# Performance work log

Measured on AMD Instinct MI355X. Metric: run time of the kernel, lower is better.

The kernel has to match this reference:

```python
import jax, jax.numpy as jnp
import numpy as np

B, L, KNN = 8, 512, 16
D, H, NL, DLAT = 1024, 16, 2, 64
DH = D // H
DFF = 4 * D
HENC = D // 2          # SwiGLUFFNEncoder hidden = d_model // 2
POS_CLIP = 32
NPOS = 2 * POS_CLIP + 1


def _layernorm(x, g, b, eps=1e-5):
    m = x.mean(-1, keepdims=True)
    v = ((x - m) ** 2).mean(-1, keepdims=True)
    return (x - m) / jnp.sqrt(v + eps) * g + b


def setup_inputs() -> dict:
    key = jax.random.key(0)
    ks = jax.random.split(key, 16)

    def g(i, shape, scale=0.02):
        return jax.random.normal(ks[i], shape, dtype=jnp.float32) * scale

    return {
        "coords": jax.random.normal(ks[0], (B, L, 3, 3), dtype=jnp.float32) * 3.0,
        "eps": jax.random.normal(ks[1], (B, L, DLAT), dtype=jnp.float32),
        "emb": g(2, (NPOS, D)),
        "ln1_g": jnp.ones((NL, D)), "ln1_b": jnp.zeros((NL, D)),
        "Wqkv": g(3, (NL, D, 3 * D)), "bqkv": jnp.zeros((NL, 3 * D)),
        "dist_scale": g(4, (NL, H), 1.0),
        "Wo": g(5, (NL, D, D)), "bo": jnp.zeros((NL, D)),
        "ln2_g": jnp.ones((NL, D)), "ln2_b": jnp.zeros((NL, D)),
        "Wf1": g(6, (NL, D, 2 * DFF)), "bf1": jnp.zeros((NL, 2 * DFF)),
        "Wf2": g(7, (NL, DFF, D)), "bf2": jnp.zeros((NL, D)),
        "lnf_g": jnp.ones((D,)), "lnf_b": jnp.zeros((D,)),
        "We1": g(8, (D, 2 * HENC)), "be1": jnp.zeros((2 * HENC,)),
        "We2": g(9, (HENC, 2 * DLAT)), "be2": jnp.zeros((2 * DLAT,)),
        "attention_mask": jnp.ones((B, L), dtype=bool),
        "sequence_id": jnp.zeros((B, L), dtype=jnp.int32),
    }


def reference(coords, eps, emb, ln1_g, ln1_b, Wqkv, bqkv, dist_scale, Wo, bo,
              ln2_g, ln2_b, Wf1, bf1, Wf2, bf2, lnf_g, lnf_b, We1, be1, We2, be2,
              attention_mask, sequence_id):
    # --- frames: only CA translations feed the geometric attention bias ---
    t = coords[..., 1, :]                       # CA atoms, [B,L,3]

    # --- KNN graph build (no_grad in torch -> stop_gradient) ---
    ca = jax.lax.stop_gradient(t)
    d2 = ((ca[:, :, None, :] - ca[:, None, :, :]) ** 2).sum(-1)   # [B,L,L]
    same_seq = sequence_id[:, :, None] == sequence_id[:, None, :]
    valid = attention_mask[:, None, :] & same_seq
    d2 = jnp.where(valid, d2, jnp.inf)
    _, edges = jax.lax.top_k(-d2, KNN)          # [B,L,KNN]; self is index 0

    def gather(x):  # node_gather: x [B,L,...] -> [B,L,KNN,...]
        return jax.vmap(lambda xb, ib: xb[ib])(x, edges)

    tg = gather(t).reshape(B * L, KNN, 3)                 # neighbor translations
    maskg = gather(attention_mask).reshape(B * L, KNN)

    # --- relative positional embedding (residue_index=None -> knn edges) ---
    res_idxs = edges.reshape(B * L, KNN)
    diff = res_idxs - res_idxs[:, :1]
    z = emb[jnp.clip(diff, -POS_CLIP, POS_CLIP) + POS_CLIP]   # [N,E,D]

    # --- local geometric transformer over the 16-neighbor window ---
    dist = jnp.sqrt(((tg[:, :, None, :] - tg[:, None, :, :]) ** 2).sum(-1) + 1e-8)  # [N,E,E]
    for l in range(NL):
        h = _layernorm(z, ln1_g[l], ln1_b[l])
        qkv = h @ Wqkv[l] + bqkv[l]
        q, k, v = [a.reshape(B * L, KNN, H, DH) for a in jnp.split(qkv, 3, axis=-1)]
        scores = jnp.einsum('nehd,nfhd->nhef', q, k) / np.sqrt(DH).astype(np.float32)
        scores = scores - jax.nn.softplus(dist_scale[l])[None, :, None, None] * dist[:, None]
        scores = jnp.where(maskg[:, None, None, :], scores, -1e9)
        a = jax.nn.softmax(scores, axis=-1)
        o = jnp.einsum('nhef,nfhd->nehd', a, v).reshape(B * L, KNN, D)
        z = z + o @ Wo[l] + bo[l]
        h2 = _layernorm(z, ln2_g[l], ln2_b[l])
        a1, b1 = jnp.split(h2 @ Wf1[l] + bf1[l], 2, axis=-1)
        z = z + (jax.nn.silu(a1) * b1) @ Wf2[l] + bf2[l]

    # --- extract central node, norm, SwiGLU encoder head, reparameterize ---
    zc = z.reshape(B, L, KNN, D)[:, :, 0, :]
    zc = _layernorm(zc, lnf_g, lnf_b)
    zc = jnp.where(attention_mask[..., None], zc, 0.0)
    u1, v1 = jnp.split(zc @ We1 + be1, 2, axis=-1)
    hh = jax.nn.silu(u1) * v1
    mu, logvar = jnp.split(hh @ We2 + be2, 2, axis=-1)
    logvar = jnp.minimum(logvar, 5.0)
    zs = mu + eps * jnp.exp(0.5 * logvar)
    return zs, mu, logvar
```

## Files before the change

kernel.cpp:

```cpp
#include <hip/hip_runtime.h>
#include <hip/hip_bf16.h>
#include <math.h>

#define LLEN 512
#define KNNK 16
#define DIM 1024
#define NHEAD 16
#define NLAYER 2
#define DFFN 4096
#define POSCLIP 32
#define NQ 4096
#define NTOK 65536
#define HSPLIT 4

typedef __attribute__((ext_vector_type(8))) short short8v;
typedef __attribute__((ext_vector_type(4))) float f32x4;
typedef unsigned short ushort_t;

__device__ __forceinline__ float b2f(ushort_t u) {
  union { unsigned u; float f; } x; x.u = ((unsigned)u) << 16; return x.f;
}

__device__ __forceinline__ void xcd_map(int bid, int Mtiles, int Ntiles, int XN,
                                        int& mt, int& nt) {
  int nt_per = Ntiles / XN;
  int mt_per = (Mtiles * XN) >> 3;
  int xcd = bid & 7, i = bid >> 3;
  int xn = xcd % XN, xm = xcd / XN;
  int ntl = i % nt_per, mtl = i / nt_per;
  mt = xm * mt_per + mtl;
  nt = xn * nt_per + ntl;
}

#define GLD16(gp, lp)                                                          \
  __builtin_amdgcn_global_load_lds(                                            \
      (const __attribute__((address_space(1))) void*)(gp),                     \
      (__attribute__((address_space(3))) void*)(lp), 16, 0, 0)

__global__ __launch_bounds__(64) void knn_kernel(const float* __restrict__ coords,
                                                 int* __restrict__ edges) {
  int n = blockIdx.x;
  int b = n / LLEN, i = n % LLEN;
  int lane = threadIdx.x;
  const float* cb = coords + (size_t)b * LLEN * 9;
  float xi = cb[i * 9 + 3], yi = cb[i * 9 + 4], zi = cb[i * 9 + 5];
  float d[8];
#pragma unroll
  for (int r = 0; r < 8; ++r) {
    int j = r * 64 + lane;
    float dx = xi - cb[j * 9 + 3];
    float dy = yi - cb[j * 9 + 4];
    float dz = zi - cb[j * 9 + 5];
    d[r] = dx * dx + dy * dy + dz * dz;
  }
  for (int s = 0; s < KNNK; ++s) {
    float bv = INFINITY; int bi = 1 << 30;
#pragma unroll
    for (int r = 0; r < 8; ++r) {
      int j = r * 64 + lane;
      if (d[r] < bv || (d[r] == bv && j < bi)) { bv = d[r]; bi = j; }
    }
#pragma unroll
    for (int off = 32; off > 0; off >>= 1) {
      float ov = __shfl_xor(bv, off);
      int   oi = __shfl_xor(bi, off);
      if (ov < bv || (ov == bv && oi < bi)) { bv = ov; bi = oi; }
    }
    if (lane == 0) edges[n * KNNK + s] = bi;
    if ((bi & 63) == lane) d[bi >> 6] = INFINITY;
  }
}

__global__ __launch_bounds__(256) void dist_kernel(const float* __restrict__ coords,
                                                   const int* __restrict__ edges,
                                                   float* __restrict__ dist) {
  int n = blockIdx.x; int b = n / LLEN;
  __shared__ float tx[16], ty[16], tz[16];
  int t = threadIdx.x;
  const float* cb = coords + (size_t)b * LLEN * 9;
  if (t < 16) {
    int j = edges[n * KNNK + t];
    tx[t] = cb[j * 9 + 3]; ty[t] = cb[j * 9 + 4]; tz[t] = cb[j * 9 + 5];
  }
  __syncthreads();
  int e = t >> 4, f = t & 15;
  float dx = tx[e] - tx[f], dy = ty[e] - ty[f], dz = tz[e] - tz[f];
  dist[(size_t)n * 256 + t] = sqrtf(dx * dx + dy * dy + dz * dz + 1e-8f);
}

__global__ __launch_bounds__(256) void zinit_kernel(const int* __restrict__ edges,
                                                    const float* __restrict__ emb,
                                                    float* __restrict__ zbuf, int tok0) {
  int tl = blockIdx.x;
  int tok = tok0 + tl;
  int n = tok >> 4;
  int diff = edges[tok] - edges[n << 4];
  int idx = min(max(diff, -POSCLIP), POSCLIP) + POSCLIP;
  ((float4*)(zbuf + (size_t)tl * DIM))[threadIdx.x] =
      ((const float4*)(emb + (size_t)idx * DIM))[threadIdx.x];
}

__global__ __launch_bounds__(256) void ln_kernel(const float* __restrict__ X, int stride,
                                                 const float* __restrict__ g,
                                                 const float* __restrict__ bta,
                                                 __hip_bfloat16* __restrict__ Y) {
  int row = blockIdx.x; int t = threadIdx.x;
  const float4* xr = (const float4*)(X + (size_t)row * stride);
  float4 v = xr[t];
  float s = v.x + v.y + v.z + v.w;
  __shared__ float red[8];
  for (int off = 32; off; off >>= 1) s += __shfl_down(s, off);
  int wid = t >> 6;
  if ((t & 63) == 0) red[wid] = s;
  __syncthreads();
  if (t == 0) red[4] = (red[0] + red[1] + red[2] + red[3]) * (1.0f / DIM);
  __syncthreads();
  float mean = red[4];
  float d0 = v.x - mean, d1 = v.y - mean, d2 = v.z - mean, d3 = v.w - mean;
  float s2 = d0 * d0 + d1 * d1 + d2 * d2 + d3 * d3;
  for (int off = 32; off; off >>= 1) s2 += __shfl_down(s2, off);
  if ((t & 63) == 0) red[wid] = s2;
  __syncthreads();
  if (t == 0) red[5] = rsqrtf((red[0] + red[1] + red[2] + red[3]) * (1.0f / DIM) + 1e-5f);
  __syncthreads();
  float rstd = red[5];
  float4 gv = ((const float4*)g)[t], bv = ((const float4*)bta)[t];
  size_t o = (size_t)row * DIM + t * 4;
  Y[o + 0] = __float2bfloat16(d0 * rstd * gv.x + bv.x);
  Y[o + 1] = __float2bfloat16(d1 * rstd * gv.y + bv.y);
  Y[o + 2] = __float2bfloat16(d2 * rstd * gv.z + bv.z);
  Y[o + 3] = __float2bfloat16(d3 * rstd * gv.w + bv.w);
}

__global__ __launch_bounds__(256) void wconv_kernel(const float* __restrict__ W,
                                                    __hip_bfloat16* __restrict__ Wt,
                                                    int K, int N) {
  __shared__ float tile[32][33];
  int n0 = blockIdx.x * 32, k0 = blockIdx.y * 32;
  int c = threadIdx.x & 31, r = threadIdx.x >> 5;
#pragma unroll
  for (int i = 0; i < 4; ++i)
    tile[r + i * 8][c] = W[(size_t)(k0 + r + i * 8) * N + n0 + c];
  __syncthreads();
#pragma unroll
  for (int i = 0; i < 4; ++i)
    Wt[(size_t)(n0 + r + i * 8) * K + k0 + c] = __float2bfloat16(tile[c][r + i * 8]);
}


template <int MODE>
__global__ __launch_bounds__(256, 3) void gemmT128_kernel(
    const ushort_t* __restrict__ A,
    const ushort_t* __restrict__ Wt,
    const float* __restrict__ bias,
    void* __restrict__ Cout,
    int K, int Mtiles, int Cstride, int Ntiles, int XN) {
  __shared__ ushort_t Alds[3][4096];
  __shared__ ushort_t Blds[3][4096];
  int t = threadIdx.x;
  int w = t >> 6, lane = t & 63;
  int wr = w >> 1, wc = w & 1;
  int fr = lane & 15, kg = lane >> 4;

  int mt, nt;
  xcd_map(blockIdx.x, Mtiles, Ntiles, XN, mt, nt);
  size_t m0 = (size_t)mt * 128, n0 = (size_t)nt * 128;

  int stg_r = w * 16 + (lane >> 2);
  int stg_c = (((lane & 3) ^ ((lane >> 3) & 3)) << 3);
  const ushort_t* gAl = A + (m0 + stg_r) * (size_t)K + stg_c;
  const ushort_t* gBl = Wt + (n0 + stg_r) * (size_t)K + stg_c;
  int lds_w = w * 512;

#define SAt(slot, kcol, j) GLD16(gAl + (size_t)(j) * 64 * K + (kcol), Alds[slot] + (j) * 2048 + lds_w)
#define SBt(slot, kcol, j) GLD16(gBl + (size_t)(j) * 64 * K + (kcol), Blds[slot] + (j) * 2048 + lds_w)

  f32x4 acc[4][4];
#pragma unroll
  for (int i = 0; i < 4; ++i)
#pragma unroll
    for (int j = 0; j < 4; ++j) acc[i][j] = (f32x4){0.f, 0.f, 0.f, 0.f};

  int usw = ((kg ^ ((fr >> 1) & 3)) << 3);

  SAt(0, 0, 0); SAt(0, 0, 1); SBt(0, 0, 0); SBt(0, 0, 1);
  SAt(1, 32, 0); SAt(1, 32, 1); SBt(1, 32, 0); SBt(1, 32, 1);
  asm volatile("s_waitcnt vmcnt(4)" ::: "memory");
  __builtin_amdgcn_s_barrier();

  short8v af[4], bf[4];
  int NT = K >> 5;
  int sl = 0, st = 2;
  for (int ti = 0; ti < NT; ++ti) {
    int kS = (ti + 2) << 5;
    int stg = (ti + 2) < NT;
    const ushort_t* sA = Alds[sl];
    const ushort_t* sB = Blds[sl];
#pragma unroll
    for (int mi = 0; mi < 4; ++mi)
      af[mi] = *(const short8v*)(sA + (wr * 64 + mi * 16 + fr) * 32 + usw);
#pragma unroll
    for (int ni = 0; ni < 4; ++ni)
      bf[ni] = *(const short8v*)(sB + (wc * 64 + ni * 16 + fr) * 32 + usw);
    if (stg) { SAt(st, kS, 0); SAt(st, kS, 1); SBt(st, kS, 0); SBt(st, kS, 1); }
    asm volatile("s_waitcnt lgkmcnt(0)" ::: "memory");
    __builtin_amdgcn_sched_barrier(0);
    __builtin_amdgcn_s_setprio(1);
#pragma unroll
    for (int mi = 0; mi < 4; ++mi)
#pragma unroll
      for (int ni = 0; ni < 4; ++ni)
        acc[mi][ni] = __builtin_amdgcn_mfma_f32_16x16x32_bf16(af[mi], bf[ni], acc[mi][ni], 0, 0, 0);
    __builtin_amdgcn_s_setprio(0);
    if (stg) { asm volatile("s_waitcnt vmcnt(4)" ::: "memory"); }
    else if (ti + 1 < NT) { asm volatile("s_waitcnt vmcnt(0)" ::: "memory"); }
    __builtin_amdgcn_s_barrier();
    sl = (sl == 2) ? 0 : sl + 1;
    st = (st == 2) ? 0 : st + 1;
  }
#undef SAt
#undef SBt

  int er = wr * 64 + (lane >> 4) * 4;
  int ec = wc * 64 + fr;
#pragma unroll
  for (int mi = 0; mi < 4; ++mi) {
#pragma unroll
    for (int ni = 0; ni < 4; ++ni) {
      int col = (int)n0 + ec + ni * 16;
      float bs = bias[col];
#pragma unroll
      for (int j = 0; j < 4; ++j) {
        size_t row = m0 + er + mi * 16 + j;
        size_t cidx = row * (size_t)Cstride + col;
        float x = acc[mi][ni][j] + bs;
        if constexpr (MODE == 0) {
          ((__hip_bfloat16*)Cout)[cidx] = __float2bfloat16(x);
        } else {
          ((float*)Cout)[cidx] += x;
        }
      }
    }
  }
}

__global__ __launch_bounds__(256, 2) void gemmGW_kernel(
    const ushort_t* __restrict__ A,
    const ushort_t* __restrict__ Wt,
    const float* __restrict__ bias,
    __hip_bfloat16* __restrict__ Cout,
    int K, int Mtiles, int Cstride, int NhRows, int Ntiles, int XN) {
  __shared__ ushort_t Alds[3][4096];
  __shared__ ushort_t B1lds[3][4096];
  __shared__ ushort_t B2lds[3][4096];
  int t = threadIdx.x;
  int w = t >> 6, lane = t & 63;
  int wr = w >> 1, wc = w & 1;
  int fr = lane & 15, kg = lane >> 4;

  int mt, nt;
  xcd_map(blockIdx.x, Mtiles, Ntiles, XN, mt, nt);
  size_t m0 = (size_t)mt * 128, n0 = (size_t)nt * 128;

  int stg_r = w * 16 + (lane >> 2);
  int stg_c = (((lane & 3) ^ ((lane >> 3) & 3)) << 3);
  const ushort_t* gAl = A + (m0 + stg_r) * (size_t)K + stg_c;
  const ushort_t* gB1 = Wt + (n0 + stg_r) * (size_t)K + stg_c;
  const ushort_t* gB2 = Wt + ((size_t)NhRows + n0 + stg_r) * (size_t)K + stg_c;
  int lds_w = w * 512;

#define SAg(slot, kcol, j) GLD16(gAl + (size_t)(j) * 64 * K + (kcol), Alds[slot] + (j) * 2048 + lds_w)
#define SB1g(slot, kcol, j) GLD16(gB1 + (size_t)(j) * 64 * K + (kcol), B1lds[slot] + (j) * 2048 + lds_w)
#define SB2g(slot, kcol, j) GLD16(gB2 + (size_t)(j) * 64 * K + (kcol), B2lds[slot] + (j) * 2048 + lds_w)

  f32x4 acc1[4][4], acc2[4][4];
#pragma unroll
  for (int i = 0; i < 4; ++i)
#pragma unroll
    for (int j = 0; j < 4; ++j) {
      acc1[i][j] = (f32x4){0.f, 0.f, 0.f, 0.f};
      acc2[i][j] = (f32x4){0.f, 0.f, 0.f, 0.f};
    }

  int usw = ((kg ^ ((fr >> 1) & 3)) << 3);

  SAg(0, 0, 0); SAg(0, 0, 1); SB1g(0, 0, 0); SB1g(0, 0, 1); SB2g(0, 0, 0); SB2g(0, 0, 1);
  SAg(1, 32, 0); SAg(1, 32, 1); SB1g(1, 32, 0); SB1g(1, 32, 1); SB2g(1, 32, 0); SB2g(1, 32, 1);
  asm volatile("s_waitcnt vmcnt(6)" ::: "memory");
  __builtin_amdgcn_s_barrier();

  short8v af[4], bf1[4], bf2[4];
  int NT = K >> 5;
  int sl = 0, st = 2;
  for (int ti = 0; ti < NT; ++ti) {
    int kS = (ti + 2) << 5;
    int stg = (ti + 2) < NT;
    const ushort_t* sA = Alds[sl];
    const ushort_t* sB1 = B1lds[sl];
    const ushort_t* sB2 = B2lds[sl];
#pragma unroll
    for (int mi = 0; mi < 4; ++mi)
      af[mi] = *(const short8v*)(sA + (wr * 64 + mi * 16 + fr) * 32 + usw);
#pragma unroll
    for (int ni = 0; ni < 4; ++ni) {
      bf1[ni] = *(const short8v*)(sB1 + (wc * 64 + ni * 16 + fr) * 32 + usw);
      bf2[ni] = *(const short8v*)(sB2 + (wc * 64 + ni * 16 + fr) * 32 + usw);
    }
    if (stg) {
      SAg(st, kS, 0); SAg(st, kS, 1);
      SB1g(st, kS, 0); SB1g(st, kS, 1);
      SB2g(st, kS, 0); SB2g(st, kS, 1);
    }
    asm volatile("s_waitcnt lgkmcnt(0)" ::: "memory");
    __builtin_amdgcn_sched_barrier(0);
    __builtin_amdgcn_s_setprio(1);
#pragma unroll
    for (int mi = 0; mi < 4; ++mi)
#pragma unroll
      for (int ni = 0; ni < 4; ++ni) {
        acc1[mi][ni] = __builtin_amdgcn_mfma_f32_16x16x32_bf16(af[mi], bf1[ni], acc1[mi][ni], 0, 0, 0);
        acc2[mi][ni] = __builtin_amdgcn_mfma_f32_16x16x32_bf16(af[mi], bf2[ni], acc2[mi][ni], 0, 0, 0);
      }
    __builtin_amdgcn_s_setprio(0);
    if (stg) { asm volatile("s_waitcnt vmcnt(6)" ::: "memory"); }
    else if (ti + 1 < NT) { asm volatile("s_waitcnt vmcnt(0)" ::: "memory"); }
    __builtin_amdgcn_s_barrier();
    sl = (sl == 2) ? 0 : sl + 1;
    st = (st == 2) ? 0 : st + 1;
  }
#undef SAg
#undef SB1g
#undef SB2g

  int er = wr * 64 + (lane >> 4) * 4;
  int ec = wc * 64 + fr;
#pragma unroll
  for (int mi = 0; mi < 4; ++mi) {
#pragma unroll
    for (int ni = 0; ni < 4; ++ni) {
      int col = (int)n0 + ec + ni * 16;
      float b1v = bias[col];
      float b2v = bias[NhRows + col];
#pragma unroll
      for (int j = 0; j < 4; ++j) {
        size_t row = m0 + er + mi * 16 + j;
        float x1 = acc1[mi][ni][j] + b1v;
        float x2 = acc2[mi][ni][j] + b2v;
        float sg = x1 / (1.f + expf(-x1));
        Cout[row * (size_t)Cstride + col] = __float2bfloat16(sg * x2);
      }
    }
  }
}

template <int MODE>
__global__ __launch_bounds__(256) void mgemm_kernel(
    const __hip_bfloat16* __restrict__ A,
    const __hip_bfloat16* __restrict__ Wt,
    const float* __restrict__ bias,
    void* __restrict__ Cout,
    int K, int Nh, int Cstride) {
  __shared__ ushort_t As[4 * 128 * 8];
  __shared__ ushort_t Bs[4 * 128 * 8];
  __shared__ ushort_t Bs2[(MODE == 2) ? 4 * 128 * 8 : 8];
  int t = threadIdx.x;
  int w = t >> 6, lane = t & 63;
  int wr = w >> 1, wc = w & 1;
  size_t m0 = (size_t)blockIdx.y * 128;
  size_t n0 = (size_t)blockIdx.x * 128;
  int cell0 = w * 64 + lane;
  int cell1 = 256 + w * 64 + lane;
  int kg0 = cell0 >> 7, rw0 = cell0 & 127;
  int kg1 = cell1 >> 7, rw1 = cell1 & 127;
  const ushort_t* gA = (const ushort_t*)A;
  const ushort_t* gB = (const ushort_t*)Wt;
  const ushort_t* gB2 = (const ushort_t*)(Wt + (size_t)Nh * K);
  size_t a0 = (m0 + rw0) * (size_t)K + kg0 * 8;
  size_t a1 = (m0 + rw1) * (size_t)K + kg1 * 8;
  size_t b0 = (n0 + rw0) * (size_t)K + kg0 * 8;
  size_t b1 = (n0 + rw1) * (size_t)K + kg1 * 8;
  int ldso0 = w * 1024;
  int ldso1 = 4096 + w * 1024;
  f32x4 acc[4][4];
  f32x4 acc2[4][4];
#pragma unroll
  for (int i = 0; i < 4; ++i)
#pragma unroll
    for (int j = 0; j < 4; ++j) {
      acc[i][j] = (f32x4){0.f, 0.f, 0.f, 0.f};
      acc2[i][j] = (f32x4){0.f, 0.f, 0.f, 0.f};
    }
  int fr = lane & 15, kg = lane >> 4;
  int abase = (kg * 128 + wr * 64 + fr) * 16;
  int bbase = (kg * 128 + wc * 64 + fr) * 16;
  for (int k0 = 0; k0 < K; k0 += 32) {
    __syncthreads();
    GLD16(gA + a0 + k0, (char*)As + ldso0);
    GLD16(gA + a1 + k0, (char*)As + ldso1);
    GLD16(gB + b0 + k0, (char*)Bs + ldso0);
    GLD16(gB + b1 + k0, (char*)Bs + ldso1);
    if constexpr (MODE == 2) {
      GLD16(gB2 + b0 + k0, (char*)Bs2 + ldso0);
      GLD16(gB2 + b1 + k0, (char*)Bs2 + ldso1);
    }
    __syncthreads();
    short8v a[4], b[4];
#pragma unroll
    for (int mi = 0; mi < 4; ++mi)
      a[mi] = *(const short8v*)((const char*)As + abase + mi * 256);
#pragma unroll
    for (int ni = 0; ni < 4; ++ni)
      b[ni] = *(const short8v*)((const char*)Bs + bbase + ni * 256);
#pragma unroll
    for (int mi = 0; mi < 4; ++mi)
#pragma unroll
      for (int ni = 0; ni < 4; ++ni)
        acc[mi][ni] = __builtin_amdgcn_mfma_f32_16x16x32_bf16(a[mi], b[ni], acc[mi][ni], 0, 0, 0);
    if constexpr (MODE == 2) {
#pragma unroll
      for (int ni = 0; ni < 4; ++ni)
        b[ni] = *(const short8v*)((const char*)Bs2 + bbase + ni * 256);
#pragma unroll
      for (int mi = 0; mi < 4; ++mi)
#pragma unroll
        for (int ni = 0; ni < 4; ++ni)
          acc2[mi][ni] = __builtin_amdgcn_mfma_f32_16x16x32_bf16(a[mi], b[ni], acc2[mi][ni], 0, 0, 0);
    }
  }
  int er = wr * 64 + (lane >> 4) * 4;
  int ec = wc * 64 + fr;
#pragma unroll
  for (int mi = 0; mi < 4; ++mi) {
#pragma unroll
    for (int ni = 0; ni < 4; ++ni) {
      int col = (int)n0 + ec + ni * 16;
      float bs1 = bias[col];
#pragma unroll
      for (int j = 0; j < 4; ++j) {
        size_t row = m0 + er + mi * 16 + j;
        size_t cidx = row * (size_t)Cstride + col;
        float x = acc[mi][ni][j] + bs1;
        if constexpr (MODE == 3) {
          ((float*)Cout)[cidx] = x;
        } else {
          float x2 = acc2[mi][ni][j] + bias[Nh + col];
          float sig = 1.f / (1.f + expf(-x));
          ((__hip_bfloat16*)Cout)[cidx] = __float2bfloat16(x * sig * x2);
        }
      }
    }
  }
}

__global__ __launch_bounds__(256) void attn_g_kernel(const __hip_bfloat16* __restrict__ qkv65,
                                                     const int* __restrict__ edges,
                                                     const float* __restrict__ dist,
                                                     const float* __restrict__ ds_l,
                                                     __hip_bfloat16* __restrict__ o) {
  int nq = blockIdx.x >> 2;
  int h0 = (blockIdx.x & 3) * (NHEAD / HSPLIT);
  int t = threadIdx.x;
  __shared__ float qs[16][65], ks[16][65], vs[16][65];
  __shared__ float sc[16][17], dl[16][17];
  __shared__ float sps_s[NHEAD];
  __shared__ int map_s[16];
  dl[t >> 4][t & 15] = dist[(size_t)nq * 256 + t];
  if (t < NHEAD) sps_s[t] = log1pf(expf(ds_l[t]));
  if (t < 16) {
    int diff = edges[nq * 16 + t] - edges[nq * 16];
    map_s[t] = min(max(diff, -POSCLIP), POSCLIP) + POSCLIP;
  }
  __syncthreads();
  int e = t >> 4, c4 = (t & 15) * 4;
  const ushort_t* qp = (const ushort_t*)qkv65;
  size_t ebase = (size_t)map_s[e] * 3072;
  for (int h = h0; h < h0 + NHEAD / HSPLIT; ++h) {
    const ushort_t* p = qp + ebase + h * 64 + c4;
    ushort4 qv = *(const ushort4*)p;
    ushort4 kv = *(const ushort4*)(p + 1024);
    ushort4 vv = *(const ushort4*)(p + 2048);
    qs[e][c4] = b2f(qv.x); qs[e][c4 + 1] = b2f(qv.y); qs[e][c4 + 2] = b2f(qv.z); qs[e][c4 + 3] = b2f(qv.w);
    ks[e][c4] = b2f(kv.x); ks[e][c4 + 1] = b2f(kv.y); ks[e][c4 + 2] = b2f(kv.z); ks[e][c4 + 3] = b2f(kv.w);
    vs[e][c4] = b2f(vv.x); vs[e][c4 + 1] = b2f(vv.y); vs[e][c4 + 2] = b2f(vv.z); vs[e][c4 + 3] = b2f(vv.w);
    __syncthreads();
    int ee = t >> 4, ff = t & 15;
    float s = 0.f;
#pragma unroll
    for (int d = 0; d < 64; ++d) s = fmaf(qs[ee][d], ks[ff][d], s);
    sc[ee][ff] = s * 0.125f - sps_s[h] * dl[ee][ff];
    __syncthreads();
    if (t < 16) {
      float m = -1e30f;
      for (int f = 0; f < 16; ++f) m = fmaxf(m, sc[t][f]);
      float sum = 0.f;
      for (int f = 0; f < 16; ++f) { float pe = expf(sc[t][f] - m); sc[t][f] = pe; sum += pe; }
      float inv = 1.f / sum;
      for (int f = 0; f < 16; ++f) sc[t][f] *= inv;
    }
    __syncthreads();
#pragma unroll
    for (int r = 0; r < 4; ++r) {
      int idx = t + 256 * r;
      int oe = idx >> 6, od = idx & 63;
      float acc = 0.f;
#pragma unroll
      for (int f = 0; f < 16; ++f) acc = fmaf(sc[oe][f], vs[f][od], acc);
      o[(size_t)(nq * 16 + oe) * 1024 + h * 64 + od] = __float2bfloat16(acc);
    }
    __syncthreads();
  }
}

__global__ __launch_bounds__(256) void attn2_kernel(const __hip_bfloat16* __restrict__ qkv,
                                                    const float* __restrict__ dist,
                                                    const float* __restrict__ ds_l,
                                                    __hip_bfloat16* __restrict__ o) {
  int nq = blockIdx.x;
  int t = threadIdx.x;
  __shared__ ushort_t ks[16 * 1032];
  __shared__ ushort_t vs[16 * 1032];
  __shared__ float qsf[1024];
  __shared__ float sc[16][17];
  __shared__ float pm[16], pi[16], sps_s[16], dl[16];
  const ushort_t* qp = (const ushort_t*)qkv;
  size_t base = (size_t)nq * 16 * 3072;
#pragma unroll
  for (int i = 0; i < 8; ++i) {
    int flat8 = (i * 256 + t) * 8;
    int e = flat8 >> 10, cc = flat8 & 1023;
    *(short8v*)(ks + e * 1032 + cc) = *(const short8v*)(qp + base + (size_t)e * 3072 + 1024 + cc);
    *(short8v*)(vs + e * 1032 + cc) = *(const short8v*)(qp + base + (size_t)e * 3072 + 2048 + cc);
  }
  {
    ushort4 qv = *(const ushort4*)(qp + base + t * 4);
    qsf[t * 4 + 0] = b2f(qv.x); qsf[t * 4 + 1] = b2f(qv.y);
    qsf[t * 4 + 2] = b2f(qv.z); qsf[t * 4 + 3] = b2f(qv.w);
  }
  if (t < 16) {
    sps_s[t] = log1pf(expf(ds_l[t]));
    dl[t] = dist[(size_t)nq * 256 + t];
  }
  __syncthreads();
  int h = t >> 4, f = t & 15;
  float s = 0.f;
#pragma unroll
  for (int dc = 0; dc < 8; ++dc) {
    short8v k8 = *(const short8v*)(ks + f * 1032 + h * 64 + dc * 8);
#pragma unroll
    for (int j = 0; j < 8; ++j)
      s = fmaf(qsf[h * 64 + dc * 8 + j], b2f((ushort_t)k8[j]), s);
  }
  sc[h][f] = s * 0.125f - sps_s[h] * dl[f];
  __syncthreads();
  if (t < 16) {
    float m = -1e30f;
    for (int ff = 0; ff < 16; ++ff) m = fmaxf(m, sc[t][ff]);
    float sum = 0.f;
    for (int ff = 0; ff < 16; ++ff) sum += expf(sc[t][ff] - m);
    pm[t] = m; pi[t] = 1.f / sum;
  }
  __syncthreads();
  float p = expf(sc[h][f] - pm[h]) * pi[h];
  __syncthreads();
  sc[h][f] = p;
  __syncthreads();
#pragma unroll
  for (int r = 0; r < 4; ++r) {
    int idx = t + 256 * r;
    int oh = idx >> 6, od = idx & 63;
    float acc = 0.f;
#pragma unroll
    for (int f2 = 0; f2 < 16; ++f2)
      acc = fmaf(sc[oh][f2], b2f(vs[f2 * 1032 + oh * 64 + od]), acc);
    o[(size_t)nq * 1024 + idx] = __float2bfloat16(acc);
  }
}

__global__ __launch_bounds__(256) void z0copy_kernel(const float* __restrict__ z,
                                                     float* __restrict__ z0) {
  ((float4*)(z0 + (size_t)blockIdx.x * 1024))[threadIdx.x] =
      ((const float4*)(z + (size_t)blockIdx.x * 16384))[threadIdx.x];
}

__global__ __launch_bounds__(64) void final_kernel(const float* __restrict__ tmp,
                                                   const float* __restrict__ eps,
                                                   float* __restrict__ out) {
  int r = blockIdx.x; int j = threadIdx.x;
  float mu = tmp[r * 128 + j];
  float lv = fminf(tmp[r * 128 + 64 + j], 5.0f);
  float zs = mu + eps[r * 64 + j] * expf(0.5f * lv);
  out[r * 64 + j] = zs;
  out[262144 + r * 64 + j] = mu;
  out[524288 + r * 64 + j] = lv;
}

extern "C" void kernel_launch(void* const* d_in, const int* in_sizes, int n_in,
                              void* d_out, int out_size, void* d_ws, size_t ws_size,
                              hipStream_t stream) {
  (void)in_sizes; (void)n_in; (void)out_size;
  const float* coords = (const float*)d_in[0];
  const float* eps    = (const float*)d_in[1];
  const float* emb    = (const float*)d_in[2];
  const float* ln1_g  = (const float*)d_in[3];
  const float* ln1_b  = (const float*)d_in[4];
  const float* Wqkv   = (const float*)d_in[5];
  const float* bqkv   = (const float*)d_in[6];
  const float* dist_scale = (const float*)d_in[7];
  const float* Wo     = (const float*)d_in[8];
  const float* bo     = (const float*)d_in[9];
  const float* ln2_g  = (const float*)d_in[10];
  const float* ln2_b  = (const float*)d_in[11];
  const float* Wf1    = (const float*)d_in[12];
  const float* bf1    = (const float*)d_in[13];
  const float* Wf2    = (const float*)d_in[14];
  const float* bf2    = (const float*)d_in[15];
  const float* lnf_g  = (const float*)d_in[16];
  const float* lnf_b  = (const float*)d_in[17];
  const float* We1    = (const float*)d_in[18];
  const float* be1    = (const float*)d_in[19];
  const float* We2    = (const float*)d_in[20];
  const float* be2    = (const float*)d_in[21];

  char* ws = (char*)d_ws;
  int*   edges = (int*)ws;
  float* dist  = (float*)(ws + (4ull << 20));
  __hip_bfloat16* hfinal = (__hip_bfloat16*)(ws + (8ull << 20));
  __hip_bfloat16* gated  = (__hip_bfloat16*)(ws + (16ull << 20));
  float* tmp   = (float*)(ws + (20ull << 20));
  __hip_bfloat16* o_all  = (__hip_bfloat16*)(ws + (22ull << 20));
  float* z0_all = (float*)(ws + (30ull << 20));
  __hip_bfloat16* wbase = (__hip_bfloat16*)(ws + (46ull << 20));
  size_t woff = 0;
  __hip_bfloat16* wqkvT = wbase + woff; woff += 2ull * 3072 * 1024;
  __hip_bfloat16* woT   = wbase + woff; woff += 2ull * 1024 * 1024;
  __hip_bfloat16* wf1T  = wbase + woff; woff += 2ull * 8192 * 1024;
  __hip_bfloat16* wf2T  = wbase + woff; woff += 2ull * 1024 * 4096;
  __hip_bfloat16* we1T  = wbase + woff; woff += 1024ull * 1024;
  __hip_bfloat16* we2T  = wbase + woff; woff += 128ull * 512;
  __hip_bfloat16* h65   = wbase + woff; woff += 128ull * 1024;
  __hip_bfloat16* qkv65 = wbase + woff; woff += 128ull * 3072;

  const size_t FIXED = 116ull << 20;
  int CQ = 4096;
  while (CQ > 256 && FIXED + (size_t)CQ * 16 * 14336ull > ws_size) CQ >>= 1;
  if (FIXED + (size_t)CQ * 16 * 14336ull > ws_size) return;
  size_t CT = (size_t)CQ * KNNK;
  char* creg = ws + FIXED;
  float* zbuf = (float*)creg;
  __hip_bfloat16* hbuf = (__hip_bfloat16*)(creg + CT * 4096);
  __hip_bfloat16* sh8  = (__hip_bfloat16*)(creg + CT * 6144);
  __hip_bfloat16* h2        = hbuf;
  __hip_bfloat16* gated_all = sh8;

  knn_kernel<<<NQ, 64, 0, stream>>>(coords, edges);
  dist_kernel<<<NQ, 256, 0, stream>>>(coords, edges, dist);
  for (int l = 0; l < NLAYER; ++l) {
    wconv_kernel<<<dim3(96, 32), 256, 0, stream>>>(Wqkv + (size_t)l * 1024 * 3072,
                                                   wqkvT + (size_t)l * 3072 * 1024, 1024, 3072);
    wconv_kernel<<<dim3(32, 32), 256, 0, stream>>>(Wo + (size_t)l * 1024 * 1024,
                                                   woT + (size_t)l * 1024 * 1024, 1024, 1024);
    wconv_kernel<<<dim3(256, 32), 256, 0, stream>>>(Wf1 + (size_t)l * 1024 * 8192,
                                                    wf1T + (size_t)l * 8192 * 1024, 1024, 8192);
    wconv_kernel<<<dim3(32, 128), 256, 0, stream>>>(Wf2 + (size_t)l * 4096 * 1024,
                                                    wf2T + (size_t)l * 1024 * 4096, 4096, 1024);
  }
  wconv_kernel<<<dim3(32, 32), 256, 0, stream>>>(We1, we1T, 1024, 1024);
  wconv_kernel<<<dim3(4, 16), 256, 0, stream>>>(We2, we2T, 512, 128);

  ln_kernel<<<65, 256, 0, stream>>>(emb, DIM, ln1_g, ln1_b, h65);
  gemmT128_kernel<0><<<24, 256, 0, stream>>>(
      (const ushort_t*)h65, (const ushort_t*)wqkvT, bqkv, qkv65, 1024, 1, 3072, 24, 8);

  int NCH = NQ / CQ;
  int MT128 = (int)(CT / 128);
  for (int c = 0; c < NCH; ++c) {
    zinit_kernel<<<(int)CT, 256, 0, stream>>>(edges, emb, zbuf, (int)(c * CT));
    attn_g_kernel<<<CQ * HSPLIT, 256, 0, stream>>>(qkv65, edges + (size_t)c * CQ * 16,
                                                   dist + (size_t)c * CQ * 256,
                                                   dist_scale, hbuf);
    gemmT128_kernel<1><<<MT128 * 8, 256, 0, stream>>>(
        (const ushort_t*)hbuf, (const ushort_t*)woT, bo, zbuf, 1024, MT128, 1024, 8, 2);
    ln_kernel<<<(int)CT, 256, 0, stream>>>(zbuf, DIM, ln2_g, ln2_b, hbuf);
    gemmGW_kernel<<<MT128 * 32, 256, 0, stream>>>(
        (const ushort_t*)hbuf, (const ushort_t*)wf1T, bf1, sh8, 1024, MT128, 4096, 4096, 32, 4);
    gemmT128_kernel<1><<<MT128 * 8, 256, 0, stream>>>(
        (const ushort_t*)sh8, (const ushort_t*)wf2T, bf2, zbuf, 4096, MT128, 1024, 8, 2);
    ln_kernel<<<(int)CT, 256, 0, stream>>>(zbuf, DIM, ln1_g + DIM, ln1_b + DIM, hbuf);
    gemmT128_kernel<0><<<MT128 * 24, 256, 0, stream>>>(
        (const ushort_t*)hbuf, (const ushort_t*)(wqkvT + 3072ull * 1024),
        bqkv + 3072, sh8, 1024, MT128, 3072, 24, 4);
    attn2_kernel<<<CQ, 256, 0, stream>>>(sh8, dist + (size_t)c * CQ * 256,
                                         dist_scale + NHEAD, o_all + (size_t)c * CQ * 1024);
    z0copy_kernel<<<CQ, 256, 0, stream>>>(zbuf, z0_all + (size_t)c * CQ * 1024);
  }

  int MTQ = NQ / 128;
  gemmT128_kernel<1><<<MTQ * 8, 256, 0, stream>>>(
      (const ushort_t*)o_all, (const ushort_t*)(woT + 1024ull * 1024),
      bo + DIM, z0_all, 1024, MTQ, 1024, 8, 2);
  ln_kernel<<<NQ, 256, 0, stream>>>(z0_all, DIM, ln2_g + DIM, ln2_b + DIM, h2);
  gemmGW_kernel<<<MTQ * 32, 256, 0, stream>>>(
      (const ushort_t*)h2, (const ushort_t*)(wf1T + 8192ull * 1024),
      bf1 + 2 * DFFN, gated_all, 1024, MTQ, 4096, 4096, 32, 4);
  gemmT128_kernel<1><<<MTQ * 8, 256, 0, stream>>>(
      (const ushort_t*)gated_all, (const ushort_t*)(wf2T + 1024ull * 4096),
      bf2 + DIM, z0_all, 4096, MTQ, 1024, 8, 2);
  ln_kernel<<<NQ, 256, 0, stream>>>(z0_all, DIM, lnf_g, lnf_b, hfinal);

  mgemm_kernel<2><<<dim3(4, 32), 256, 0, stream>>>(hfinal, we1T, be1, gated, 1024, 512, 512);
  mgemm_kernel<3><<<dim3(1, 32), 256, 0, stream>>>(gated, we2T, be2, tmp, 512, 0, 128);
  final_kernel<<<NQ, 64, 0, stream>>>(tmp, eps, (float*)d_out);
}
```

Baseline: 3.536 ms.

## Compute layer-2 Q only for center tokens and fuse z init into Wo GEMM epilogue

In the second layer only the central node's output is needed, so the QKV projection is split: K/V are computed for all tokens, while Q is computed only for the center token of each neighborhood. A small copy gathers the center rows for that separate Q GEMM. Separately, the zinit kernel is removed and the positional embedding gather is folded into a new Wo GEMM epilogue mode that writes emb + result instead of accumulating. This cuts about a third of the layer-2 QKV GEMM FLOPs and removes one full pass over zbuf, at the cost of an extra small GEMM launch and scattered embedding reads in the epilogue.

```diff
diff --git a/kernel.cpp b/kernel.cpp
--- a/kernel.cpp
+++ b/kernel.cpp
@@ -86,18 +86,6 @@
   int e = t >> 4, f = t & 15;
   float dx = tx[e] - tx[f], dy = ty[e] - ty[f], dz = tz[e] - tz[f];
   dist[(size_t)n * 256 + t] = sqrtf(dx * dx + dy * dy + dz * dz + 1e-8f);
-}
-
-__global__ __launch_bounds__(256) void zinit_kernel(const int* __restrict__ edges,
-                                                    const float* __restrict__ emb,
-                                                    float* __restrict__ zbuf, int tok0) {
-  int tl = blockIdx.x;
-  int tok = tok0 + tl;
-  int n = tok >> 4;
-  int diff = edges[tok] - edges[n << 4];
-  int idx = min(max(diff, -POSCLIP), POSCLIP) + POSCLIP;
-  ((float4*)(zbuf + (size_t)tl * DIM))[threadIdx.x] =
-      ((const float4*)(emb + (size_t)idx * DIM))[threadIdx.x];
 }
 
 __global__ __launch_bounds__(256) void ln_kernel(const float* __restrict__ X, int stride,
@@ -154,7 +142,8 @@
     const ushort_t* __restrict__ Wt,
     const float* __restrict__ bias,
     void* __restrict__ Cout,
-    int K, int Mtiles, int Cstride, int Ntiles, int XN) {
+    int K, int Mtiles, int Cstride, int Ntiles, int XN,
+    const int* __restrict__ eg, const float* __restrict__ embg, int tok0) {
   __shared__ ushort_t Alds[3][4096];
   __shared__ ushort_t Blds[3][4096];
   int t = threadIdx.x;
@@ -236,8 +225,14 @@
         float x = acc[mi][ni][j] + bs;
         if constexpr (MODE == 0) {
           ((__hip_bfloat16*)Cout)[cidx] = __float2bfloat16(x);
+        } else if constexpr (MODE == 1) {
+          ((float*)Cout)[cidx] += x;
         } else {
-          ((float*)Cout)[cidx] += x;
+          int tok = tok0 + (int)row;
+          int n = tok >> 4;
+          int diff = eg[tok] - eg[n << 4];
+          int idx = min(max(diff, -POSCLIP), POSCLIP) + POSCLIP;
+          ((float*)Cout)[cidx] = embg[(size_t)idx * DIM + col] + x;
         }
       }
     }
@@ -511,7 +506,14 @@
   }
 }
 
-__global__ __launch_bounds__(256) void attn2_kernel(const __hip_bfloat16* __restrict__ qkv,
+__global__ __launch_bounds__(256) void h0copy_kernel(const __hip_bfloat16* __restrict__ h,
+                                                     __hip_bfloat16* __restrict__ hq) {
+  ((ushort4*)((ushort_t*)hq + (size_t)blockIdx.x * 1024))[threadIdx.x] =
+      ((const ushort4*)((const ushort_t*)h + (size_t)blockIdx.x * 16384))[threadIdx.x];
+}
+
+__global__ __launch_bounds__(256) void attn2_kernel(const __hip_bfloat16* __restrict__ qbuf,
+                                                    const __hip_bfloat16* __restrict__ kv,
                                                     const float* __restrict__ dist,
                                                     const float* __restrict__ ds_l,
                                                     __hip_bfloat16* __restrict__ o) {
@@ -522,17 +524,17 @@
   __shared__ float qsf[1024];
   __shared__ float sc[16][17];
   __shared__ float pm[16], pi[16], sps_s[16], dl[16];
-  const ushort_t* qp = (const ushort_t*)qkv;
-  size_t base = (size_t)nq * 16 * 3072;
+  const ushort_t* kvp = (const ushort_t*)kv;
+  size_t kvb = (size_t)nq * 16 * 2048;
 #pragma unroll
   for (int i = 0; i < 8; ++i) {
     int flat8 = (i * 256 + t) * 8;
     int e = flat8 >> 10, cc = flat8 & 1023;
-    *(short8v*)(ks + e * 1032 + cc) = *(const short8v*)(qp + base + (size_t)e * 3072 + 1024 + cc);
-    *(short8v*)(vs + e * 1032 + cc) = *(const short8v*)(qp + base + (size_t)e * 3072 + 2048 + cc);
+    *(short8v*)(ks + e * 1032 + cc) = *(const short8v*)(kvp + kvb + (size_t)e * 2048 + cc);
+    *(short8v*)(vs + e * 1032 + cc) = *(const short8v*)(kvp + kvb + (size_t)e * 2048 + 1024 + cc);
   }
   {
-    ushort4 qv = *(const ushort4*)(qp + base + t * 4);
+    ushort4 qv = *(const ushort4*)((const ushort_t*)qbuf + (size_t)nq * 1024 + t * 4);
     qsf[t * 4 + 0] = b2f(qv.x); qsf[t * 4 + 1] = b2f(qv.y);
     qsf[t * 4 + 2] = b2f(qv.z); qsf[t * 4 + 3] = b2f(qv.w);
   }
@@ -649,6 +651,8 @@
   float* zbuf = (float*)creg;
   __hip_bfloat16* hbuf = (__hip_bfloat16*)(creg + CT * 4096);
   __hip_bfloat16* sh8  = (__hip_bfloat16*)(creg + CT * 6144);
+  __hip_bfloat16* hq   = sh8 + (size_t)CT * 2048;
+  __hip_bfloat16* qbuf = hq + (size_t)CQ * 1024;
   __hip_bfloat16* h2        = hbuf;
   __hip_bfloat16* gated_all = sh8;
 
@@ -669,27 +673,35 @@
 
   ln_kernel<<<65, 256, 0, stream>>>(emb, DIM, ln1_g, ln1_b, h65);
   gemmT128_kernel<0><<<24, 256, 0, stream>>>(
-      (const ushort_t*)h65, (const ushort_t*)wqkvT, bqkv, qkv65, 1024, 1, 3072, 24, 8);
+      (const ushort_t*)h65, (const ushort_t*)wqkvT, bqkv, qkv65, 1024, 1, 3072, 24, 8,
+      nullptr, nullptr, 0);
 
   int NCH = NQ / CQ;
   int MT128 = (int)(CT / 128);
+  int MTQc = CQ / 128;
+  int XNq = (MTQc >= 8) ? 1 : (8 / MTQc);
   for (int c = 0; c < NCH; ++c) {
-    zinit_kernel<<<(int)CT, 256, 0, stream>>>(edges, emb, zbuf, (int)(c * CT));
     attn_g_kernel<<<CQ * HSPLIT, 256, 0, stream>>>(qkv65, edges + (size_t)c * CQ * 16,
                                                    dist + (size_t)c * CQ * 256,
                                                    dist_scale, hbuf);
-    gemmT128_kernel<1><<<MT128 * 8, 256, 0, stream>>>(
-        (const ushort_t*)hbuf, (const ushort_t*)woT, bo, zbuf, 1024, MT128, 1024, 8, 2);
+    gemmT128_kernel<4><<<MT128 * 8, 256, 0, stream>>>(
+        (const ushort_t*)hbuf, (const ushort_t*)woT, bo, zbuf, 1024, MT128, 1024, 8, 2,
+        edges, emb, (int)(c * CT));
     ln_kernel<<<(int)CT, 256, 0, stream>>>(zbuf, DIM, ln2_g, ln2_b, hbuf);
     gemmGW_kernel<<<MT128 * 32, 256, 0, stream>>>(
         (const ushort_t*)hbuf, (const ushort_t*)wf1T, bf1, sh8, 1024, MT128, 4096, 4096, 32, 4);
     gemmT128_kernel<1><<<MT128 * 8, 256, 0, stream>>>(
-        (const ushort_t*)sh8, (const ushort_t*)wf2T, bf2, zbuf, 4096, MT128, 1024, 8, 2);
+        (const ushort_t*)sh8, (const ushort_t*)wf2T, bf2, zbuf, 4096, MT128, 1024, 8, 2,
+        nullptr, nullptr, 0);
     ln_kernel<<<(int)CT, 256, 0, stream>>>(zbuf, DIM, ln1_g + DIM, ln1_b + DIM, hbuf);
-    gemmT128_kernel<0><<<MT128 * 24, 256, 0, stream>>>(
-        (const ushort_t*)hbuf, (const ushort_t*)(wqkvT + 3072ull * 1024),
-        bqkv + 3072, sh8, 1024, MT128, 3072, 24, 4);
-    attn2_kernel<<<CQ, 256, 0, stream>>>(sh8, dist + (size_t)c * CQ * 256,
+    gemmT128_kernel<0><<<MT128 * 16, 256, 0, stream>>>(
+        (const ushort_t*)hbuf, (const ushort_t*)(wqkvT + 3072ull * 1024 + 1024ull * 1024),
+        bqkv + 3072 + 1024, sh8, 1024, MT128, 2048, 16, 4, nullptr, nullptr, 0);
+    h0copy_kernel<<<CQ, 256, 0, stream>>>(hbuf, hq);
+    gemmT128_kernel<0><<<MTQc * 8, 256, 0, stream>>>(
+        (const ushort_t*)hq, (const ushort_t*)(wqkvT + 3072ull * 1024),
+        bqkv + 3072, qbuf, 1024, MTQc, 1024, 8, XNq, nullptr, nullptr, 0);
+    attn2_kernel<<<CQ, 256, 0, stream>>>(qbuf, sh8, dist + (size_t)c * CQ * 256,
                                          dist_scale + NHEAD, o_all + (size_t)c * CQ * 1024);
     z0copy_kernel<<<CQ, 256, 0, stream>>>(zbuf, z0_all + (size_t)c * CQ * 1024);
   }
@@ -697,14 +709,14 @@
   int MTQ = NQ / 128;
   gemmT128_kernel<1><<<MTQ * 8, 256, 0, stream>>>(
       (const ushort_t*)o_all, (const ushort_t*)(woT + 1024ull * 1024),
-      bo + DIM, z0_all, 1024, MTQ, 1024, 8, 2);
+      bo + DIM, z0_all, 1024, MTQ, 1024, 8, 2, nullptr, nullptr, 0);
   ln_kernel<<<NQ, 256, 0, stream>>>(z0_all, DIM, ln2_g + DIM, ln2_b + DIM, h2);
   gemmGW_kernel<<<MTQ * 32, 256, 0, stream>>>(
       (const ushort_t*)h2, (const ushort_t*)(wf1T + 8192ull * 1024),
       bf1 + 2 * DFFN, gated_all, 1024, MTQ, 4096, 4096, 32, 4);
   gemmT128_kernel<1><<<MTQ * 8, 256, 0, stream>>>(
       (const ushort_t*)gated_all, (const ushort_t*)(wf2T + 1024ull * 4096),
-      bf2 + DIM, z0_all, 4096, MTQ, 1024, 8, 2);
+      bf2 + DIM, z0_all, 4096, MTQ, 1024, 8, 2, nullptr, nullptr, 0);
   ln_kernel<<<NQ, 256, 0, stream>>>(z0_all, DIM, lnf_g, lnf_b, hfinal);
 
   mgemm_kernel<2><<<dim3(4, 32), 256, 0, stream>>>(hfinal, we1T, be1, gated, 1024, 512, 512);
```

After: 3.404 ms. 3.7% less time.
